# Kernel tuning notes

Measured on AMD Instinct MI355X. Metric: run time of the kernel, lower is better.

## Reference

```python
import jax, jax.numpy as jnp
import numpy as np

ETA = 0.1      # eta detuning in the 'experiment' dynamics
NT = 5         # integrator steps
DT = 0.5 / NT  # dt = t_end / Nt
DIM1 = 14 * 14        # 196
DIM2 = 14 * 14 + 10   # 206
BATCH = 65536


def c2q(C):
    # symmetrize, then overwrite diagonal with negative column sums
    Q = 0.5 * (C + C.T)
    d = -jnp.sum(Q, axis=0)
    n = Q.shape[0]
    idx = jnp.arange(n)
    return Q.at[idx, idx].set(d)


def ode_exp(z, Q, e, Qn):
    # 'experiment' dynamics: detuned sin + structured noise coupling Qn
    q, p = z[..., 0], z[..., 1]
    sq = jnp.sin((1.0 + ETA) * q)
    dp = -sq + e + sq @ Q + sq @ Qn
    return jnp.stack([p, dp], axis=-1)


def ode_model(z, Q, e):
    # differentiable model dynamics
    q, p = z[..., 0], z[..., 1]
    sq = jnp.sin(q)
    dp = -sq + e + sq @ Q
    return jnp.stack([p, dp], axis=-1)


def ode_map(f, z, *args):
    # explicit Euler, Nt steps (small fixed loop, unrolled)
    for _ in range(NT):
        z = z + DT * f(z, *args)
    return z


def pat(z, C, e, Qn):
    # physics-aware training: forward = experiment, gradient = model
    Q = c2q(C)
    zm = ode_map(ode_model, z, Q, e)
    ze = ode_map(lambda zz, Q_, e_: ode_exp(zz, Q_, e_, Qn), z, Q, e)
    return zm + jax.lax.stop_gradient(ze - zm)


def setup_inputs() -> dict:
    key = jax.random.key(0)
    ks = jax.random.split(key, 8)
    s1 = 1.0 / np.sqrt(DIM1)
    s2 = 1.0 / np.sqrt(DIM2)
    x = jax.random.normal(ks[0], (BATCH, DIM1), dtype=jnp.float32)
    fc1_w = jax.random.uniform(ks[1], (DIM1, DIM1), jnp.float32, -s1, s1)
    fc1_b = jax.random.uniform(ks[2], (DIM1,), jnp.float32, -s1, s1)
    fc2_w = jax.random.uniform(ks[3], (DIM2, DIM2), jnp.float32, -s2, s2)
    fc2_b = jax.random.uniform(ks[4], (DIM2,), jnp.float32, -s2, s2)
    Q_noise_small = c2q(0.2 * jax.random.normal(ks[5], (DIM1, DIM1), dtype=jnp.float32))
    Q_noise_large = c2q(0.2 * jax.random.normal(ks[6], (DIM2, DIM2), dtype=jnp.float32))
    output_fac = jnp.float32(1.0)
    return {"x": x, "fc1_w": fc1_w, "fc1_b": fc1_b, "fc2_w": fc2_w,
            "fc2_b": fc2_b, "output_fac": output_fac,
            "Q_noise_small": Q_noise_small, "Q_noise_large": Q_noise_large}


def reference(x, fc1_w, fc1_b, fc2_w, fc2_b, output_fac, Q_noise_small, Q_noise_large):
    B = x.shape[0]
    # stage 1: [B,196,2] state, PAT-integrated with fc1 weights
    z = jnp.stack([x, jnp.zeros_like(x)], axis=-1)
    z = pat(z, fc1_w, fc1_b, Q_noise_small)
    q = z[..., 0]
    # stage 2: pad with 10 class nodes -> [B,206,2]
    z = jnp.stack([q, jnp.zeros_like(q)], axis=-1)
    z = jnp.concatenate([z, jnp.zeros((B, 10, 2), dtype=x.dtype)], axis=1)
    z = pat(z, fc2_w, fc2_b, Q_noise_large)
    return output_fac * z[:, -10:, 0]
```

## Files before the change

kernel.cpp:

```cpp
#include <hip/hip_runtime.h>
#include <hip/hip_bf16.h>
#include <stdint.h>


typedef __attribute__((ext_vector_type(8))) short bh8;
typedef __attribute__((ext_vector_type(4))) float f32x4;

#define TILES 13
#define KSTEPS 7
#define ROWDW 128
#define BROWS 32
#define BUFDW (BROWS * ROWDW)

static __device__ __forceinline__ uint16_t bf16_bits(float v) {
    __hip_bfloat16 h = __float2bfloat16(v);
    return *reinterpret_cast<uint16_t*>(&h);
}

__global__ void prep_diag(const float* __restrict__ C1,
                          const float* __restrict__ C2,
                          float* __restrict__ d) {
    const int bid = blockIdx.x;
    const int st = bid >> 8 ? 1 : (bid >= 208);
    const int j = bid - st * 208;
    const float* C = st ? C2 : C1;
    const int N = st ? 206 : 196;
    if (j >= N) return;
    const int t = threadIdx.x;
    float s = 0.f;
    for (int i = t; i < N; i += 64)
        s += 0.5f * (C[i * N + j] + C[j * N + i]);
    #pragma unroll
    for (int off = 32; off > 0; off >>= 1)
        s += __shfl_xor(s, off, 64);
    if (t == 0) d[st * 208 + j] = -s;
}

__global__ void pack_frags(const float* __restrict__ C1, const float* __restrict__ Qn1,
                           const float* __restrict__ e1,
                           const float* __restrict__ C2, const float* __restrict__ Qn2,
                           const float* __restrict__ e2,
                           const float* __restrict__ diag,
                           uint16_t* __restrict__ frag) {
    const int bid = blockIdx.x;
    const int st = bid / (TILES * KSTEPS);
    const int rem = bid - st * (TILES * KSTEPS);
    const int tile = rem / KSTEPS, ks = rem % KSTEPS;
    const float* C  = st ? C2 : C1;
    const float* Qn = st ? Qn2 : Qn1;
    const float* e  = st ? e2 : e1;
    const float* dd = diag + st * 208;
    const int N = st ? 206 : 196;
    const int lane = threadIdx.x;
    const int quad = (lane >> 4) & 3;
    const int n = tile * 16 + (lane & 15);
    union { uint16_t v16[8]; uint4 v128; } vals;
    #pragma unroll
    for (int j = 0; j < 8; ++j) {
        const int k = ks * 32 + quad * 8 + j;
        float v = 0.f;
        if (n < N) {
            if (k < N) {
                if (k == n) v = dd[n] + Qn[n * N + n] - 1.0f;
                else        v = 0.5f * (C[k * N + n] + C[n * N + k]) + Qn[k * N + n];
                v *= 0.1f;
            } else if (k == 208) {
                v = 0.1f * e[n];
            }
        }
        vals.v16[j] = bf16_bits(v);
    }
    const size_t off = ((size_t)(st * TILES + tile) * KSTEPS + ks) * 64 + lane;
    reinterpret_cast<uint4*>(frag)[off] = vals.v128;
}

__global__ __launch_bounds__(512, 4) void pat_main(
    const float* __restrict__ x, const uint16_t* __restrict__ frag,
    const float* __restrict__ fac, float* __restrict__ out) {
    __shared__ __align__(16) uint32_t sinb[3 * BUFDW];
    const int tid = threadIdx.x;
    const int lane = tid & 63;
    const int w = __builtin_amdgcn_readfirstlane(tid >> 6);
    const int c = lane & 15, quad = lane >> 4;
    const uint32_t cs = (uint32_t)(c & 7);
    const long batch0 = (long)blockIdx.x * BROWS + c;
    const int t0 = w, t1 = w + 8;
    const int ntiles = (w < 5) ? 2 : 1;

    {
        uint4 z; z.x = 0; z.y = 0; z.z = 0; z.w = 0;
        #pragma unroll
        for (int i = 0; i < 6; ++i)
            reinterpret_cast<uint4*>(sinb)[tid + i * 512] = z;
    }

    const bh8* fragv = reinterpret_cast<const bh8*>(frag);
    bh8 A[2][KSTEPS];
    #pragma unroll
    for (int nt = 0; nt < 2; ++nt)
        if (nt < ntiles) {
            const int tile = nt ? t1 : t0;
            #pragma unroll
            for (int ks = 0; ks < KSTEPS; ++ks)
                A[nt][ks] = fragv[((size_t)tile * KSTEPS + ks) * 64 + lane];
        }

    float q[2][2][4];
    f32x4 P[2][2];
    #pragma unroll
    for (int nt = 0; nt < 2; ++nt) {
        const int n0 = (nt ? t1 : t0) * 16 + quad * 4;
        #pragma unroll
        for (int bt = 0; bt < 2; ++bt) {
            const long batch = batch0 + bt * 16;
            if (nt < ntiles && n0 + 3 < 196) {
                const float4 v = *reinterpret_cast<const float4*>(x + batch * 196 + n0);
                q[nt][bt][0] = v.x; q[nt][bt][1] = v.y;
                q[nt][bt][2] = v.z; q[nt][bt][3] = v.w;
            } else {
                #pragma unroll
                for (int r = 0; r < 4; ++r) q[nt][bt][r] = 0.f;
            }
            #pragma unroll
            for (int r = 0; r < 4; ++r) P[nt][bt][r] = 0.f;
        }
    }
    const float fout = fac[0];

    auto sin_phase = [&](int buf) {
        #pragma unroll
        for (int nt = 0; nt < 2; ++nt)
            if (nt < ntiles) {
                const int tile = nt ? t1 : t0;
                const uint32_t blk = ((uint32_t)(tile * 2 + (quad >> 1))) ^ cs;
                #pragma unroll
                for (int bt = 0; bt < 2; ++bt) {
                    uint2 u;
                    u.x = (uint32_t)bf16_bits(__sinf(1.1f * q[nt][bt][0]))
                        | ((uint32_t)bf16_bits(__sinf(1.1f * q[nt][bt][1])) << 16);
                    u.y = (uint32_t)bf16_bits(__sinf(1.1f * q[nt][bt][2]))
                        | ((uint32_t)bf16_bits(__sinf(1.1f * q[nt][bt][3])) << 16);
                    *reinterpret_cast<uint2*>(
                        &sinb[buf * BUFDW + (c + bt * 16) * ROWDW
                              + blk * 4 + (quad & 1) * 2]) = u;
                }
            }
    };
    auto mfma_phase = [&](int buf) {
        #pragma unroll
        for (int ks = 0; ks < KSTEPS; ++ks) {
            const uint32_t koff = (((uint32_t)(ks * 4 + quad)) ^ cs) * 4;
            const bh8 b0 = *reinterpret_cast<const bh8*>(
                &sinb[buf * BUFDW + c * ROWDW + koff]);
            const bh8 b1 = *reinterpret_cast<const bh8*>(
                &sinb[buf * BUFDW + (c + 16) * ROWDW + koff]);
            #pragma unroll
            for (int nt = 0; nt < 2; ++nt)
                if (nt < ntiles) {
                    P[nt][0] = __builtin_amdgcn_mfma_f32_16x16x32_bf16(A[nt][ks], b0, P[nt][0], 0, 0, 0);
                    P[nt][1] = __builtin_amdgcn_mfma_f32_16x16x32_bf16(A[nt][ks], b1, P[nt][1], 0, 0, 0);
                }
        }
    };
    auto q_update = [&]() {
        #pragma unroll
        for (int nt = 0; nt < 2; ++nt)
            if (nt < ntiles)
                #pragma unroll
                for (int bt = 0; bt < 2; ++bt)
                    #pragma unroll
                    for (int r = 0; r < 4; ++r)
                        q[nt][bt][r] += 0.1f * P[nt][bt][r];
    };

    __syncthreads();
    if (tid < 96) {
        const int bb = tid >> 5, cc = tid & 31;
        sinb[bb * BUFDW + cc * ROWDW + (26u ^ (uint32_t)(cc & 7)) * 4] = 0x3F80u;
    }
    sin_phase(0);
    __syncthreads();

    for (int stg = 0; stg < 2; ++stg) {
        mfma_phase(0);
        q_update();
        sin_phase(1);
        #pragma unroll
        for (int nt = 0; nt < 2; ++nt)
            #pragma unroll
            for (int bt = 0; bt < 2; ++bt)
                #pragma unroll
                for (int r = 0; r < 4; ++r)
                    P[nt][bt][r] += P[nt][bt][r];
        q_update();
        sin_phase(2);
        __syncthreads();
        mfma_phase(1);
        q_update();
        mfma_phase(2);
        if (stg == 0) {
            #pragma unroll
            for (int nt = 0; nt < 2; ++nt)
                if (nt < ntiles) {
                    const int tile = nt ? t1 : t0;
                    #pragma unroll
                    for (int ks = 0; ks < KSTEPS; ++ks)
                        A[nt][ks] = fragv[((size_t)(TILES + tile) * KSTEPS + ks) * 64 + lane];
                }
        }
        q_update();
        if (stg == 0) {
            #pragma unroll
            for (int nt = 0; nt < 2; ++nt)
                #pragma unroll
                for (int bt = 0; bt < 2; ++bt)
                    #pragma unroll
                    for (int r = 0; r < 4; ++r) P[nt][bt][r] = 0.f;
            sin_phase(0);
            __syncthreads();
        }
    }

    if (w == 4) {
        const int n0 = 192 + quad * 4;
        #pragma unroll
        for (int r = 0; r < 4; ++r) {
            const int node = n0 + r;
            if (node >= 196 && node < 206) {
                out[batch0 * 10 + (node - 196)]        = fout * q[1][0][r];
                out[(batch0 + 16) * 10 + (node - 196)] = fout * q[1][1][r];
            }
        }
    }
}

extern "C" void kernel_launch(void* const* d_in, const int* in_sizes, int n_in,
                              void* d_out, int out_size, void* d_ws, size_t ws_size,
                              hipStream_t stream) {
    const float* x   = (const float*)d_in[0];
    const float* w1  = (const float*)d_in[1];
    const float* b1  = (const float*)d_in[2];
    const float* w2  = (const float*)d_in[3];
    const float* b2  = (const float*)d_in[4];
    const float* fac = (const float*)d_in[5];
    const float* qn1 = (const float*)d_in[6];
    const float* qn2 = (const float*)d_in[7];
    float* out = (float*)d_out;

    float*    diag = (float*)d_ws;
    uint16_t* frg  = (uint16_t*)((char*)d_ws + 2048);

    prep_diag<<<416, 64, 0, stream>>>(w1, w2, diag);
    pack_frags<<<2 * TILES * KSTEPS, 64, 0, stream>>>(w1, qn1, b1, w2, qn2, b2, diag, frg);

    const int B = in_sizes[0] / 196;
    pat_main<<<B / BROWS, 512, 0, stream>>>(x, frg, fac, out);
}
```

Baseline: 135.2 us.

## Fuse diag and fragment packing kernels; use raw hardware sin with prescaled state

Merges the diagonal column-sum kernel into the fragment-packing kernel, so each block computes its tile's diagonal in shared memory and one launch replaces two. In the main kernel, the state q is kept prescaled by 1.1/(2π) so the hardware sin instruction (which takes revolutions) can be used directly, and the output factor undoes the scaling. The bf16 conversion is replaced by a cheap add-and-permute round-half-up pack. This cuts the launch count and transcendental/conversion ALU work, at the cost of slightly different rounding.

```diff
diff --git a/kernel.cpp b/kernel.cpp
--- a/kernel.cpp
+++ b/kernel.cpp
@@ -12,66 +12,81 @@
 #define BROWS 32
 #define BUFDW (BROWS * ROWDW)
 
+#define K_QR 0.17507043f
+#define K_PR 0.017507043f
+#define K_OUT 5.7119866f
+
 static __device__ __forceinline__ uint16_t bf16_bits(float v) {
     __hip_bfloat16 h = __float2bfloat16(v);
     return *reinterpret_cast<uint16_t*>(&h);
 }
 
-__global__ void prep_diag(const float* __restrict__ C1,
-                          const float* __restrict__ C2,
-                          float* __restrict__ d) {
+static __device__ __forceinline__ uint32_t pack_bf16_rh(float s0, float s1) {
+    const uint32_t u0 = __float_as_uint(s0) + 0x8000u;
+    const uint32_t u1 = __float_as_uint(s1) + 0x8000u;
+    return __builtin_amdgcn_perm(u1, u0, 0x07060302u);
+}
+
+__global__ void prep_pack(const float* __restrict__ C1, const float* __restrict__ Qn1,
+                          const float* __restrict__ e1,
+                          const float* __restrict__ C2, const float* __restrict__ Qn2,
+                          const float* __restrict__ e2,
+                          uint16_t* __restrict__ frag) {
     const int bid = blockIdx.x;
-    const int st = bid >> 8 ? 1 : (bid >= 208);
-    const int j = bid - st * 208;
-    const float* C = st ? C2 : C1;
-    const int N = st ? 206 : 196;
-    if (j >= N) return;
-    const int t = threadIdx.x;
-    float s = 0.f;
-    for (int i = t; i < N; i += 64)
-        s += 0.5f * (C[i * N + j] + C[j * N + i]);
-    #pragma unroll
-    for (int off = 32; off > 0; off >>= 1)
-        s += __shfl_xor(s, off, 64);
-    if (t == 0) d[st * 208 + j] = -s;
-}
-
-__global__ void pack_frags(const float* __restrict__ C1, const float* __restrict__ Qn1,
-                           const float* __restrict__ e1,
-                           const float* __restrict__ C2, const float* __restrict__ Qn2,
-                           const float* __restrict__ e2,
-                           const float* __restrict__ diag,
-                           uint16_t* __restrict__ frag) {
-    const int bid = blockIdx.x;
-    const int st = bid / (TILES * KSTEPS);
-    const int rem = bid - st * (TILES * KSTEPS);
-    const int tile = rem / KSTEPS, ks = rem % KSTEPS;
+    const int st = bid / TILES, tile = bid % TILES;
     const float* C  = st ? C2 : C1;
     const float* Qn = st ? Qn2 : Qn1;
     const float* e  = st ? e2 : e1;
-    const float* dd = diag + st * 208;
     const int N = st ? 206 : 196;
-    const int lane = threadIdx.x;
+    const int t = threadIdx.x;
+    __shared__ float part_col[16][17];
+    __shared__ float part_row[16][17];
+    __shared__ float dsh[16];
+    {
+        const int col = t & 15, seg = t >> 4;
+        const int n = tile * 16 + col;
+        float sc = 0.f;
+        if (n < N)
+            for (int i = seg; i < N; i += 16) sc += C[i * N + n];
+        part_col[col][seg] = sc;
+        const int row = t >> 4, ii = t & 15;
+        const int n2 = tile * 16 + row;
+        float sr = 0.f;
+        if (n2 < N)
+            for (int i = ii; i < N; i += 16) sr += C[n2 * N + i];
+        part_row[row][ii] = sr;
+    }
+    __syncthreads();
+    if (t < 16) {
+        float d = 0.f;
+        #pragma unroll
+        for (int j = 0; j < 16; ++j) d += part_col[t][j] + part_row[t][j];
+        dsh[t] = -0.5f * d;
+    }
+    __syncthreads();
+    const int lane = t & 63, grp = t >> 6;
     const int quad = (lane >> 4) & 3;
     const int n = tile * 16 + (lane & 15);
-    union { uint16_t v16[8]; uint4 v128; } vals;
-    #pragma unroll
-    for (int j = 0; j < 8; ++j) {
-        const int k = ks * 32 + quad * 8 + j;
-        float v = 0.f;
-        if (n < N) {
-            if (k < N) {
-                if (k == n) v = dd[n] + Qn[n * N + n] - 1.0f;
-                else        v = 0.5f * (C[k * N + n] + C[n * N + k]) + Qn[k * N + n];
-                v *= 0.1f;
-            } else if (k == 208) {
-                v = 0.1f * e[n];
-            }
-        }
-        vals.v16[j] = bf16_bits(v);
-    }
-    const size_t off = ((size_t)(st * TILES + tile) * KSTEPS + ks) * 64 + lane;
-    reinterpret_cast<uint4*>(frag)[off] = vals.v128;
+    for (int ks = grp; ks < KSTEPS; ks += 4) {
+        union { uint16_t v16[8]; uint4 v128; } vals;
+        #pragma unroll
+        for (int j = 0; j < 8; ++j) {
+            const int k = ks * 32 + quad * 8 + j;
+            float v = 0.f;
+            if (n < N) {
+                if (k < N) {
+                    if (k == n) v = dsh[lane & 15] + Qn[n * N + n] - 1.0f;
+                    else        v = 0.5f * (C[k * N + n] + C[n * N + k]) + Qn[k * N + n];
+                    v *= 0.1f;
+                } else if (k == 208) {
+                    v = 0.1f * e[n];
+                }
+            }
+            vals.v16[j] = bf16_bits(v);
+        }
+        const size_t off = ((size_t)(st * TILES + tile) * KSTEPS + ks) * 64 + lane;
+        reinterpret_cast<uint4*>(frag)[off] = vals.v128;
+    }
 }
 
 __global__ __launch_bounds__(512, 4) void pat_main(
@@ -115,8 +130,8 @@
             const long batch = batch0 + bt * 16;
             if (nt < ntiles && n0 + 3 < 196) {
                 const float4 v = *reinterpret_cast<const float4*>(x + batch * 196 + n0);
-                q[nt][bt][0] = v.x; q[nt][bt][1] = v.y;
-                q[nt][bt][2] = v.z; q[nt][bt][3] = v.w;
+                q[nt][bt][0] = K_QR * v.x; q[nt][bt][1] = K_QR * v.y;
+                q[nt][bt][2] = K_QR * v.z; q[nt][bt][3] = K_QR * v.w;
             } else {
                 #pragma unroll
                 for (int r = 0; r < 4; ++r) q[nt][bt][r] = 0.f;
@@ -125,7 +140,7 @@
             for (int r = 0; r < 4; ++r) P[nt][bt][r] = 0.f;
         }
     }
-    const float fout = fac[0];
+    const float fout = fac[0] * K_OUT;
 
     auto sin_phase = [&](int buf) {
         #pragma unroll
@@ -136,10 +151,10 @@
                 #pragma unroll
                 for (int bt = 0; bt < 2; ++bt) {
                     uint2 u;
-                    u.x = (uint32_t)bf16_bits(__sinf(1.1f * q[nt][bt][0]))
-                        | ((uint32_t)bf16_bits(__sinf(1.1f * q[nt][bt][1])) << 16);
-                    u.y = (uint32_t)bf16_bits(__sinf(1.1f * q[nt][bt][2]))
-                        | ((uint32_t)bf16_bits(__sinf(1.1f * q[nt][bt][3])) << 16);
+                    u.x = pack_bf16_rh(__builtin_amdgcn_sinf(q[nt][bt][0]),
+                                       __builtin_amdgcn_sinf(q[nt][bt][1]));
+                    u.y = pack_bf16_rh(__builtin_amdgcn_sinf(q[nt][bt][2]),
+                                       __builtin_amdgcn_sinf(q[nt][bt][3]));
                     *reinterpret_cast<uint2*>(
                         &sinb[buf * BUFDW + (c + bt * 16) * ROWDW
                               + blk * 4 + (quad & 1) * 2]) = u;
@@ -170,7 +185,7 @@
                 for (int bt = 0; bt < 2; ++bt)
                     #pragma unroll
                     for (int r = 0; r < 4; ++r)
-                        q[nt][bt][r] += 0.1f * P[nt][bt][r];
+                        q[nt][bt][r] += K_PR * P[nt][bt][r];
     };
 
     __syncthreads();
@@ -247,11 +262,9 @@
     const float* qn2 = (const float*)d_in[7];
     float* out = (float*)d_out;
 
-    float*    diag = (float*)d_ws;
-    uint16_t* frg  = (uint16_t*)((char*)d_ws + 2048);
-
-    prep_diag<<<416, 64, 0, stream>>>(w1, w2, diag);
-    pack_frags<<<2 * TILES * KSTEPS, 64, 0, stream>>>(w1, qn1, b1, w2, qn2, b2, diag, frg);
+    uint16_t* frg = (uint16_t*)d_ws;
+
+    prep_pack<<<2 * TILES, 256, 0, stream>>>(w1, qn1, b1, w2, qn2, b2, frg);
 
     const int B = in_sizes[0] / 196;
     pat_main<<<B / BROWS, 512, 0, stream>>>(x, frg, fac, out);
```

Result: slower. 142.4 us (+5.3%).
